# Kernel optimization log

Hardware: AMD Instinct MI355X
Metric: run time of the kernel (lower is better)

The kernel has to match this reference:

```python
import jax, jax.numpy as jnp
import numpy as np

N_NODES = 50000


def _degree_norms(edge_index, n_nodes):
    # PyG GCNConv: add self-loops, deg = 1 + in-degree at target (col)
    src, dst = edge_index[0], edge_index[1]
    deg = 1.0 + jax.ops.segment_sum(jnp.ones(src.shape[0], jnp.float32), dst,
                                    num_segments=n_nodes)
    d_inv_sqrt = 1.0 / jnp.sqrt(deg)  # deg >= 1 always (self-loop)
    norm_e = d_inv_sqrt[src] * d_inv_sqrt[dst]   # per-edge sym norm
    norm_self = d_inv_sqrt * d_inv_sqrt          # self-loop weight
    return norm_e, norm_self


def _gcn_conv(x, W, b, src, dst, norm_e, norm_self, n_nodes):
    h = x @ W                                    # [N, F_out]
    msg = h[src] * norm_e[:, None]               # gather + scale, [E, F_out]
    agg = jax.ops.segment_sum(msg, dst, num_segments=n_nodes)
    return agg + norm_self[:, None] * h + b


def setup_inputs() -> dict:
    key = jax.random.key(0)
    ks = jax.random.split(key, 10)
    F_in, H = 128, 128
    E = 1_600_000
    x = jax.random.normal(ks[0], (N_NODES, F_in), jnp.float32)
    edge_index = jax.random.randint(ks[1], (2, E), 0, N_NODES, dtype=jnp.int64)

    def glorot(k, fi, fo):
        s = jnp.sqrt(6.0 / (fi + fo)).astype(jnp.float32)
        return jax.random.uniform(k, (fi, fo), jnp.float32, -s, s)

    return {
        "x": x,
        "edge_index": edge_index,
        "W1": glorot(ks[2], F_in, H), "b1": jnp.zeros((H,), jnp.float32),
        "W2": glorot(ks[3], H, H),    "b2": jnp.zeros((H,), jnp.float32),
        "W3": glorot(ks[4], H, H),    "b3": jnp.zeros((H,), jnp.float32),
        "W4": glorot(ks[5], H, 1),    "b4": jnp.zeros((1,), jnp.float32),
    }


def reference(x, edge_index, W1, b1, W2, b2, W3, b3, W4, b4):
    src, dst = edge_index[0], edge_index[1]
    norm_e, norm_self = _degree_norms(edge_index, N_NODES)
    h = jax.nn.relu(_gcn_conv(x, W1, b1, src, dst, norm_e, norm_self, N_NODES))
    h = jax.nn.relu(_gcn_conv(h, W2, b2, src, dst, norm_e, norm_self, N_NODES))
    h = jax.nn.relu(_gcn_conv(h, W3, b3, src, dst, norm_e, norm_self, N_NODES))
    return _gcn_conv(h, W4, b4, src, dst, norm_e, norm_self, N_NODES)
```

## Files before the change

### kernel.cpp

```cpp
#include <hip/hip_runtime.h>
#include <hip/hip_bf16.h>
#include <stdint.h>

typedef unsigned int u32;
typedef unsigned short u16;

#define F 128

typedef __attribute__((ext_vector_type(8))) short bf16x8;
typedef __attribute__((ext_vector_type(8))) u16 u16x8;
typedef __attribute__((ext_vector_type(4))) float f32x4;

__device__ __forceinline__ float bf2f(u16 v){
  union { u32 u; float f; } x; x.u = ((u32)v) << 16; return x.f;
}
__device__ __forceinline__ float bflo(u32 w){
  union { u32 u; float f; } x; x.u = w << 16; return x.f;
}
__device__ __forceinline__ float bfhi(u32 w){
  union { u32 u; float f; } x; x.u = w & 0xFFFF0000u; return x.f;
}
__device__ __forceinline__ u16 f2bf(float f){
  union { float f; u32 u; } x; x.f = f;
  u32 u = x.u;
  return (u16)((u + 0x7fffu + ((u >> 16) & 1u)) >> 16);
}

__global__ void k_flags(const u32* __restrict__ xw, const u32* __restrict__ ei,
                        int* __restrict__ flags){
  if (blockIdx.x == 0){
    u32 hit = 0;
    for (int i = threadIdx.x; i < 2048; i += 256){
      u32 e = (xw[i] >> 7) & 0xFFu;
      if (e > 160u) hit = 1;
    }
    if (hit) atomicOr(&flags[1], 1);
  } else {
    u32 v = 0;
    for (int i = threadIdx.x; i < 4096; i += 256) v |= ei[2*i + 1];
    if (v) atomicOr(&flags[0], 1);
  }
}

__launch_bounds__(256)
__global__ void k_bhist(const u32* __restrict__ w, int E, const int* __restrict__ flagp,
                        int NB, int* __restrict__ bcnt){
  __shared__ int h[256];
  int st = (*flagp) ? 1 : 2;
  int t = threadIdx.x;
  h[t] = 0;
  __syncthreads();
  int base = blockIdx.x*4096;
  #pragma unroll 4
  for (int k = 0; k < 16; k++){
    int i = base + k*256 + t;
    if (i < E){
      int d = (int)w[(size_t)(E + i)*st];
      atomicAdd(&h[d >> 8], 1);
    }
  }
  __syncthreads();
  if (t < NB && h[t]) atomicAdd(&bcnt[t], h[t]);
}

__global__ void k_bscan(const int* __restrict__ bcnt, int NB, int E,
                        int* __restrict__ bbase, int* __restrict__ bump){
  __shared__ int s[256];
  int t = threadIdx.x;
  int v = (t < NB) ? bcnt[t] : 0;
  s[t] = v;
  __syncthreads();
  for (int off = 1; off < 256; off <<= 1){
    int x = (t >= off) ? s[t - off] : 0;
    __syncthreads();
    s[t] += x;
    __syncthreads();
  }
  bbase[t] = s[t] - v;
  if (t == 255) bbase[256] = E;
  bump[t] = 0;
}

__launch_bounds__(256)
__global__ void k_msplit(const u32* __restrict__ w, int E, const int* __restrict__ flagp,
                         const int* __restrict__ bbase, int* __restrict__ bump,
                         u32* __restrict__ ebuf){
  __shared__ int h[256];
  __shared__ int cb[256];
  int st = (*flagp) ? 1 : 2;
  int t = threadIdx.x;
  h[t] = 0;
  __syncthreads();
  int base = blockIdx.x*4096;
  u32 ps[16]; int bk[16]; int rk[16];
  #pragma unroll 4
  for (int k = 0; k < 16; k++){
    int i = base + k*256 + t;
    if (i < E){
      u32 s = w[(size_t)i*st];
      u32 d = w[(size_t)(E + i)*st];
      bk[k] = (int)(d >> 8);
      ps[k] = (s & 0xFFFFu) | ((d & 0xFFu) << 16);
      rk[k] = atomicAdd(&h[bk[k]], 1);
    } else bk[k] = -1;
  }
  __syncthreads();
  cb[t] = h[t] ? (bbase[t] + atomicAdd(&bump[t], h[t])) : 0;
  __syncthreads();
  #pragma unroll 4
  for (int k = 0; k < 16; k++){
    if (bk[k] >= 0) ebuf[cb[bk[k]] + rk[k]] = ps[k];
  }
}

__launch_bounds__(256)
__global__ void k_bemit(const u32* __restrict__ ebuf, const int* __restrict__ bbase,
                        int N, int* __restrict__ deg, int* __restrict__ rs,
                        u16* __restrict__ csr, float* __restrict__ dis){
  __shared__ int nd[256];
  __shared__ int nofs[256];
  __shared__ int s[256];
  int b = blockIdx.x;
  int t = threadIdx.x;
  int e0 = bbase[b], e1 = bbase[b + 1];
  nd[t] = 0;
  __syncthreads();
  for (int i = e0 + t; i < e1; i += 256) atomicAdd(&nd[ebuf[i] >> 16], 1);
  __syncthreads();
  int v = nd[t];
  s[t] = v;
  __syncthreads();
  for (int off = 1; off < 256; off <<= 1){
    int x = (t >= off) ? s[t - off] : 0;
    __syncthreads();
    s[t] += x;
    __syncthreads();
  }
  nofs[t] = s[t] - v;
  int node = b*256 + t;
  if (node < N){
    deg[node] = v;
    rs[node]  = e0 + nofs[t];
    dis[node] = rsqrtf(1.0f + (float)v);
  }
  nd[t] = 0;
  __syncthreads();
  for (int i = e0 + t; i < e1; i += 256){
    u32 p = ebuf[i];
    int d = (int)(p >> 16);
    int pos = e0 + nofs[d] + atomicAdd(&nd[d], 1);
    csr[pos] = (u16)(p & 0xFFFFu);
  }
}

__global__ void k_prep(const void* b1, const void* b2, const void* b3,
                       const void* W4, const void* b4, const int* __restrict__ isf32,
                       float* __restrict__ bb, float* __restrict__ wf4,
                       float* __restrict__ bb4){
  int t = threadIdx.x;
  int f32 = *isf32;
  if (t < 384){
    const void* s = (t < 128) ? b1 : ((t < 256) ? b2 : b3);
    int i = t & 127;
    bb[t] = f32 ? ((const float*)s)[i] : bf2f(((const u16*)s)[i]);
  } else if (t < 512){
    int i = t - 384;
    wf4[i] = f32 ? ((const float*)W4)[i] : bf2f(((const u16*)W4)[i]);
  } else if (t == 512){
    bb4[0] = f32 ? ((const float*)b4)[0] : bf2f(((const u16*)b4)[0]);
  }
}

__global__ void k_cvt_b(const void* __restrict__ in, const int* __restrict__ isf32,
                        u16* __restrict__ out, int NF8){
  int i = blockIdx.x*256 + threadIdx.x;
  if (i >= NF8) return;
  u16x8 o;
  if (*isf32){
    const f32x4* p = (const f32x4*)in + i*2;
    f32x4 v0 = p[0], v1 = p[1];
    #pragma unroll
    for (int k = 0; k < 4; k++){ o[k] = f2bf(v0[k]); o[k+4] = f2bf(v1[k]); }
  } else {
    o = *((const u16x8*)in + i);
  }
  __builtin_nontemporal_store(o, (u16x8*)out + i);
}

__global__ void k_swz3(const void* W1, const void* W2, const void* W3,
                       const int* __restrict__ isf32, u16* __restrict__ WL){
  int l = blockIdx.x >> 6;
  const void* W = (l == 0) ? W1 : ((l == 1) ? W2 : W3);
  int idx = (blockIdx.x & 63)*256 + threadIdx.x;
  int j    = idx & 7;
  int lane = (idx >> 3) & 63;
  int kb   = (idx >> 9) & 3;
  int ct   = idx >> 11;
  int m = lane & 15, q = lane >> 4;
  int k = kb*32 + q*8 + j;
  int c = ct*16 + m;
  float v = (*isf32) ? ((const float*)W)[k*F + c] : bf2f(((const u16*)W)[k*F + c]);
  WL[l*16384 + idx] = f2bf(v);
}

__launch_bounds__(256)
__global__ void k_mm(const u16* __restrict__ X, const u16* __restrict__ WL,
                     const float* __restrict__ dis, u16* __restrict__ G, int N){
  int w = threadIdx.x >> 6, lane = threadIdx.x & 63;
  int m = lane & 15, q = lane >> 4;
  int row0 = blockIdx.x*64 + w*16;
  int arow = row0 + m;
  bf16x8 a[4];
  if (arow < N){
    const u16* xp = X + (size_t)arow*F;
    #pragma unroll
    for (int kb = 0; kb < 4; kb++) a[kb] = *(const bf16x8*)(xp + kb*32 + q*8);
  } else {
    #pragma unroll
    for (int kb = 0; kb < 4; kb++) a[kb] = (bf16x8){0,0,0,0,0,0,0,0};
  }
  f32x4 acc[8];
  #pragma unroll
  for (int ct = 0; ct < 8; ct++) acc[ct] = (f32x4){0.f,0.f,0.f,0.f};
  #pragma unroll
  for (int ct = 0; ct < 8; ct++){
    #pragma unroll
    for (int kb = 0; kb < 4; kb++){
      bf16x8 b = *(const bf16x8*)(WL + ((size_t)((ct*4 + kb)*64 + lane))*8);
      acc[ct] = __builtin_amdgcn_mfma_f32_16x16x32_bf16(a[kb], b, acc[ct], 0, 0, 0);
    }
  }
  int rbase = row0 + q*4;
  #pragma unroll
  for (int r = 0; r < 4; r++){
    int row = rbase + r;
    if (row < N){
      float dv = dis[row];
      #pragma unroll
      for (int ct = 0; ct < 8; ct++)
        __builtin_nontemporal_store(f2bf(dv*acc[ct][r]),
                                    &G[(size_t)row*F + ct*16 + m]);
    }
  }
}

__launch_bounds__(256)
__global__ void k_agg(const u16* __restrict__ G, const float* __restrict__ dis,
                      const int* __restrict__ rs, const int* __restrict__ deg,
                      const u16* __restrict__ csr, const float* __restrict__ bias,
                      u16* __restrict__ Xout, int N, int relu){
  int wid  = blockIdx.x*4 + (threadIdx.x >> 6);
  int lane = threadIdx.x & 63;
  if (wid >= N) return;
  int base = rs[wid], len = deg[wid];
  const char* Gb = (const char*)G;
  u32 fo = 4u*(u32)lane;
  u32 sw = *(const u32*)(Gb + ((size_t)(u32)wid << 8) + fo);
  float a0 = bflo(sw), a1 = bfhi(sw);
  float pa[8], qa[8];
  #pragma unroll
  for (int k = 0; k < 8; k++){ pa[k] = 0.f; qa[k] = 0.f; }

  int mm = (len < 64) ? len : 64;
  u32 soff = 0;
  if (lane < mm) soff = ((u32)csr[base + lane]) << 8;
  int c0 = 0;
  while (c0 < len){
    int nxt = c0 + 64;
    u32 soff_n = 0;
    int nmm = len - nxt;
    if (nmm > 64) nmm = 64;
    if (nmm > 0 && lane < nmm) soff_n = ((u32)csr[base + nxt + lane]) << 8;
    int j = 0;
    for (; j + 8 <= mm; j += 8){
      u32 w[8];
      #pragma unroll
      for (int k = 0; k < 8; k++){
        u32 o = (u32)__builtin_amdgcn_readlane((int)soff, j + k);
        w[k] = *(const u32*)(Gb + o + fo);
      }
      #pragma unroll
      for (int k = 0; k < 8; k++){
        pa[k] += bflo(w[k]); qa[k] += bfhi(w[k]);
      }
    }
    for (; j < mm; j++){
      u32 o = (u32)__builtin_amdgcn_readlane((int)soff, j);
      u32 wv = *(const u32*)(Gb + o + fo);
      pa[0] += bflo(wv); qa[0] += bfhi(wv);
    }
    soff = soff_n; mm = nmm; c0 = nxt;
  }
  a0 += ((pa[0] + pa[1]) + (pa[2] + pa[3])) + ((pa[4] + pa[5]) + (pa[6] + pa[7]));
  a1 += ((qa[0] + qa[1]) + (qa[2] + qa[3])) + ((qa[4] + qa[5]) + (qa[6] + qa[7]));
  float dv = dis[wid];
  float o0 = fmaf(dv, a0, bias[2*lane]);
  float o1 = fmaf(dv, a1, bias[2*lane + 1]);
  if (relu){ o0 = fmaxf(o0, 0.f); o1 = fmaxf(o1, 0.f); }
  u32 pk = (u32)f2bf(o0) | ((u32)f2bf(o1) << 16);
  __builtin_nontemporal_store(pk, (u32*)(Xout + (size_t)wid*F + 2*lane));
}

__global__ void k_mm4(const u16* __restrict__ X, const float* __restrict__ W4f,
                      const float* __restrict__ dis, float* __restrict__ G4, int N){
  int gt   = blockIdx.x*blockDim.x + threadIdx.x;
  int wid  = gt >> 6;
  int lane = threadIdx.x & 63;
  if (wid >= N) return;
  u32 xw = *(const u32*)(X + (size_t)wid*F + 2*lane);
  float acc = bflo(xw)*W4f[2*lane] + bfhi(xw)*W4f[2*lane + 1];
  #pragma unroll
  for (int off = 32; off > 0; off >>= 1) acc += __shfl_down(acc, off, 64);
  if (lane == 0) G4[wid] = dis[wid]*acc;
}

__global__ void k_agg4(const float* __restrict__ G4, const float* __restrict__ dis,
                       const int* __restrict__ rs, const int* __restrict__ deg,
                       const u16* __restrict__ csr, const float* __restrict__ b4f,
                       const int* __restrict__ isf32, void* __restrict__ out, int N){
  int i = blockIdx.x*blockDim.x + threadIdx.x;
  if (i >= N) return;
  int base = rs[i], len = deg[i];
  float a0 = 0.f, a1 = 0.f, a2 = 0.f, a3 = 0.f;
  int j = 0;
  for (; j + 4 <= len; j += 4){
    int s0 = csr[base + j],     s1 = csr[base + j + 1];
    int s2 = csr[base + j + 2], s3 = csr[base + j + 3];
    a0 += G4[s0]; a1 += G4[s1]; a2 += G4[s2]; a3 += G4[s3];
  }
  for (; j < len; j++) a0 += G4[csr[base + j]];
  float r = dis[i]*(G4[i] + ((a0 + a1) + (a2 + a3))) + b4f[0];
  if (*isf32) ((float*)out)[i] = r;
  else        ((u16*)out)[i]   = f2bf(r);
}

extern "C" void kernel_launch(void* const* d_in, const int* in_sizes, int n_in,
                              void* d_out, int out_size, void* d_ws, size_t ws_size,
                              hipStream_t stream){
  const void* x0 = d_in[0];
  const u32*  ei = (const u32*)d_in[1];
  const void* Wp[4] = {d_in[2], d_in[4], d_in[6], d_in[8]};
  const void* bp[4] = {d_in[3], d_in[5], d_in[7], d_in[9]};
  int N = in_sizes[0] / F;
  int E = in_sizes[1] / 2;
  int NB = (N + 255) >> 8;

  char* base = (char*)d_ws;
  size_t off = 0;
  auto alloc = [&](size_t bytes)->char*{
    char* p = base + off;
    off = (off + bytes + 255) & ~(size_t)255;
    return p;
  };
  int*   deg  = (int*)  alloc((size_t)N*4);
  float* dis  = (float*)alloc((size_t)N*4);
  int*   rs   = (int*)  alloc((size_t)N*4);
  float* g4   = (float*)alloc((size_t)N*4);
  int*   bcnt = (int*)  alloc(1024);
  int*   bbase= (int*)  alloc(1056);
  int*   bump = (int*)  alloc(1024);
  int*   flags= (int*)  alloc(256);
  u32*   ebuf = (u32*)  alloc((size_t)E*4);
  u16*   csr  = (u16*)  alloc((size_t)E*2);
  u16*   WL   = (u16*)  alloc(3*16384*2);
  float* wf4  = (float*)alloc(F*4);
  float* bb   = (float*)alloc(3*F*4);
  float* bb4  = (float*)alloc(256);
  u16*   gbuf = (u16*)  alloc((size_t)N*F*2);
  u16*   xbuf = (u16*)  alloc((size_t)N*F*2);

  hipMemsetAsync(bcnt, 0, 1024, stream);
  hipMemsetAsync(flags, 0, 256, stream);

  int* eflag = flags + 0;
  int* isf32 = flags + 1;

  int nbt = (N + 255)/256;
  int etb = (E + 4095)/4096;

  k_flags <<<2, 256, 0, stream>>>((const u32*)x0, ei, flags);
  k_bhist <<<etb, 256, 0, stream>>>(ei, E, eflag, NB, bcnt);
  k_bscan <<<1, 256, 0, stream>>>(bcnt, NB, E, bbase, bump);
  k_msplit<<<etb, 256, 0, stream>>>(ei, E, eflag, bbase, bump, ebuf);
  k_bemit <<<NB, 256, 0, stream>>>(ebuf, bbase, N, deg, rs, csr, dis);
  k_prep  <<<1, 640, 0, stream>>>(bp[0], bp[1], bp[2], Wp[3], bp[3], isf32, bb, wf4, bb4);
  k_swz3  <<<192, 256, 0, stream>>>(Wp[0], Wp[1], Wp[2], isf32, WL);
  int NF8 = N*F/8;
  k_cvt_b <<<(NF8 + 255)/256, 256, 0, stream>>>(x0, isf32, xbuf, NF8);

  int mmb = (N + 63)/64;
  int agb = (N + 3)/4;

  for (int l = 0; l < 3; l++){
    k_mm <<<mmb, 256, 0, stream>>>(xbuf, WL + l*16384, dis, gbuf, N);
    k_agg<<<agb, 256, 0, stream>>>(gbuf, dis, rs, deg, csr, bb + l*F, xbuf, N, 1);
  }
  k_mm4 <<<((size_t)N*64 + 255)/256, 256, 0, stream>>>(xbuf, wf4, dis, g4, N);
  k_agg4<<<nbt, 256, 0, stream>>>(g4, dis, rs, deg, csr, bb4, isf32, (void*)d_out, N);
}
```

Before: 369.7 us.

## Fuse setup kernels, pad CSR rows to 16, and fold input conversion into first matmul

```diff
diff --git a/kernel.cpp b/kernel.cpp
--- a/kernel.cpp
+++ b/kernel.cpp
@@ -13,40 +13,77 @@
 
 __device__ __forceinline__ float bf2f(u16 v){
   union { u32 u; float f; } x; x.u = ((u32)v) << 16; return x.f;
-}
-__device__ __forceinline__ float bflo(u32 w){
-  union { u32 u; float f; } x; x.u = w << 16; return x.f;
-}
-__device__ __forceinline__ float bfhi(u32 w){
-  union { u32 u; float f; } x; x.u = w & 0xFFFF0000u; return x.f;
 }
 __device__ __forceinline__ u16 f2bf(float f){
   union { float f; u32 u; } x; x.f = f;
   u32 u = x.u;
   return (u16)((u + 0x7fffu + ((u >> 16) & 1u)) >> 16);
 }
-
-__global__ void k_flags(const u32* __restrict__ xw, const u32* __restrict__ ei,
-                        int* __restrict__ flags){
-  if (blockIdx.x == 0){
-    u32 hit = 0;
-    for (int i = threadIdx.x; i < 2048; i += 256){
-      u32 e = (xw[i] >> 7) & 0xFFu;
-      if (e > 160u) hit = 1;
-    }
-    if (hit) atomicOr(&flags[1], 1);
+__device__ __forceinline__ bf16x8 as_bf(u16x8 v){
+  union { u16x8 a; bf16x8 b; } u; u.a = v; return u.b;
+}
+__device__ __forceinline__ void d2(float& a, u32 w, u32 sel){
+  asm("v_dot2_f32_bf16 %0, %1, %2, %0" : "+v"(a) : "v"(w), "v"(sel));
+}
+__device__ __forceinline__ int detect_f32(const u32* xw){
+  u32 hit = 0;
+  for (int i = threadIdx.x; i < 2048; i += 256){
+    u32 e = (xw[i] >> 7) & 0xFFu;
+    if (e > 160u) hit = 1;
+  }
+  return __syncthreads_or((int)hit);
+}
+__device__ __forceinline__ int detect_stride(const u32* ei){
+  u32 v = 0;
+  for (int i = threadIdx.x; i < 4096; i += 256) v |= ei[2*i + 1];
+  return __syncthreads_or((int)v) ? 1 : 2;
+}
+
+__global__ void k_setup(const void* x0,
+                        const void* b1, const void* b2, const void* b3,
+                        const void* W1, const void* W2, const void* W3,
+                        const void* W4, const void* b4,
+                        float* __restrict__ bb, float* __restrict__ wf4,
+                        float* __restrict__ bb4, u16* __restrict__ WL,
+                        int* __restrict__ bcnt, int* __restrict__ bump,
+                        float* __restrict__ g4, u16* __restrict__ gz, int N){
+  int t = threadIdx.x, b = blockIdx.x;
+  int f32 = detect_f32((const u32*)x0);
+  if (b == 0){
+    bcnt[t] = 0; bump[t] = 0;
+    for (int i = t; i < 384; i += 256){
+      const void* s = (i < 128) ? b1 : ((i < 256) ? b2 : b3);
+      int ii = i & 127;
+      bb[i] = f32 ? ((const float*)s)[ii] : bf2f(((const u16*)s)[ii]);
+    }
+    if (t < 128) wf4[t] = f32 ? ((const float*)W4)[t] : bf2f(((const u16*)W4)[t]);
+    if (t == 0){
+      bb4[0] = f32 ? ((const float*)b4)[0] : bf2f(((const u16*)b4)[0]);
+      g4[N] = 0.f;
+    }
+    if (t < 64) ((u32*)gz)[t] = 0;
   } else {
-    u32 v = 0;
-    for (int i = threadIdx.x; i < 4096; i += 256) v |= ei[2*i + 1];
-    if (v) atomicOr(&flags[0], 1);
+    int bb_ = b - 1;
+    int l = bb_ >> 6;
+    const void* W = (l == 0) ? W1 : ((l == 1) ? W2 : W3);
+    int idx = (bb_ & 63)*256 + t;
+    int j    = idx & 7;
+    int lane = (idx >> 3) & 63;
+    int kb   = (idx >> 9) & 3;
+    int ct   = idx >> 11;
+    int m = lane & 15, q = lane >> 4;
+    int k = kb*32 + q*8 + j;
+    int c = ct*16 + m;
+    float v = f32 ? ((const float*)W)[k*F + c] : bf2f(((const u16*)W)[k*F + c]);
+    WL[l*16384 + idx] = f2bf(v);
   }
 }
 
 __launch_bounds__(256)
-__global__ void k_bhist(const u32* __restrict__ w, int E, const int* __restrict__ flagp,
-                        int NB, int* __restrict__ bcnt){
+__global__ void k_bhist(const u32* __restrict__ w, int E, int NB,
+                        int* __restrict__ bcnt){
   __shared__ int h[256];
-  int st = (*flagp) ? 1 : 2;
+  int st = detect_stride(w);
   int t = threadIdx.x;
   h[t] = 0;
   __syncthreads();
@@ -63,34 +100,26 @@
   if (t < NB && h[t]) atomicAdd(&bcnt[t], h[t]);
 }
 
-__global__ void k_bscan(const int* __restrict__ bcnt, int NB, int E,
-                        int* __restrict__ bbase, int* __restrict__ bump){
-  __shared__ int s[256];
-  int t = threadIdx.x;
-  int v = (t < NB) ? bcnt[t] : 0;
-  s[t] = v;
-  __syncthreads();
-  for (int off = 1; off < 256; off <<= 1){
-    int x = (t >= off) ? s[t - off] : 0;
-    __syncthreads();
-    s[t] += x;
-    __syncthreads();
-  }
-  bbase[t] = s[t] - v;
-  if (t == 255) bbase[256] = E;
-  bump[t] = 0;
-}
-
 __launch_bounds__(256)
-__global__ void k_msplit(const u32* __restrict__ w, int E, const int* __restrict__ flagp,
-                         const int* __restrict__ bbase, int* __restrict__ bump,
+__global__ void k_msplit(const u32* __restrict__ w, int E, int NB,
+                         const int* __restrict__ bcnt, int* __restrict__ bump,
                          u32* __restrict__ ebuf){
   __shared__ int h[256];
   __shared__ int cb[256];
-  int st = (*flagp) ? 1 : 2;
+  __shared__ int sc[256];
+  int st = detect_stride(w);
   int t = threadIdx.x;
+  int vv = (t < NB) ? bcnt[t] : 0;
+  sc[t] = vv;
   h[t] = 0;
   __syncthreads();
+  for (int off = 1; off < 256; off <<= 1){
+    int x = (t >= off) ? sc[t - off] : 0;
+    __syncthreads();
+    sc[t] += x;
+    __syncthreads();
+  }
+  int bbase = sc[t] - vv;
   int base = blockIdx.x*4096;
   u32 ps[16]; int bk[16]; int rk[16];
   #pragma unroll 4
@@ -105,7 +134,7 @@
     } else bk[k] = -1;
   }
   __syncthreads();
-  cb[t] = h[t] ? (bbase[t] + atomicAdd(&bump[t], h[t])) : 0;
+  cb[t] = h[t] ? (bbase + atomicAdd(&bump[t], h[t])) : 0;
   __syncthreads();
   #pragma unroll 4
   for (int k = 0; k < 16; k++){
@@ -114,21 +143,17 @@
 }
 
 __launch_bounds__(256)
-__global__ void k_bemit(const u32* __restrict__ ebuf, const int* __restrict__ bbase,
-                        int N, int* __restrict__ deg, int* __restrict__ rs,
-                        u16* __restrict__ csr, float* __restrict__ dis){
+__global__ void k_bemit(const u32* __restrict__ ebuf, const int* __restrict__ bcnt,
+                        int NB, int N, int* __restrict__ deg, int* __restrict__ rs,
+                        u32* __restrict__ csr32, float* __restrict__ dis){
   __shared__ int nd[256];
   __shared__ int nofs[256];
   __shared__ int s[256];
+  __shared__ int e01[2];
   int b = blockIdx.x;
   int t = threadIdx.x;
-  int e0 = bbase[b], e1 = bbase[b + 1];
-  nd[t] = 0;
-  __syncthreads();
-  for (int i = e0 + t; i < e1; i += 256) atomicAdd(&nd[ebuf[i] >> 16], 1);
-  __syncthreads();
-  int v = nd[t];
-  s[t] = v;
+  int vv = (t < NB) ? bcnt[t] : 0;
+  s[t] = vv;
   __syncthreads();
   for (int off = 1; off < 256; off <<= 1){
     int x = (t >= off) ? s[t - off] : 0;
@@ -136,11 +161,28 @@
     s[t] += x;
     __syncthreads();
   }
-  nofs[t] = s[t] - v;
+  if (t == 0){ e01[0] = (b == 0) ? 0 : s[b - 1]; e01[1] = s[b]; }
+  nd[t] = 0;
+  __syncthreads();
+  int e0 = e01[0], e1 = e01[1];
+  int pb = ((e0 + 15) & ~15) + b*4096;
+  for (int i = e0 + t; i < e1; i += 256) atomicAdd(&nd[ebuf[i] >> 16], 1);
+  __syncthreads();
+  int v = nd[t];
+  int pv = (v + 15) & ~15;
+  s[t] = pv;
+  __syncthreads();
+  for (int off = 1; off < 256; off <<= 1){
+    int x = (t >= off) ? s[t - off] : 0;
+    __syncthreads();
+    s[t] += x;
+    __syncthreads();
+  }
+  nofs[t] = s[t] - pv;
   int node = b*256 + t;
   if (node < N){
     deg[node] = v;
-    rs[node]  = e0 + nofs[t];
+    rs[node]  = pb + nofs[t];
     dis[node] = rsqrtf(1.0f + (float)v);
   }
   nd[t] = 0;
@@ -148,76 +190,49 @@
   for (int i = e0 + t; i < e1; i += 256){
     u32 p = ebuf[i];
     int d = (int)(p >> 16);
-    int pos = e0 + nofs[d] + atomicAdd(&nd[d], 1);
-    csr[pos] = (u16)(p & 0xFFFFu);
-  }
-}
-
-__global__ void k_prep(const void* b1, const void* b2, const void* b3,
-                       const void* W4, const void* b4, const int* __restrict__ isf32,
-                       float* __restrict__ bb, float* __restrict__ wf4,
-                       float* __restrict__ bb4){
-  int t = threadIdx.x;
-  int f32 = *isf32;
-  if (t < 384){
-    const void* s = (t < 128) ? b1 : ((t < 256) ? b2 : b3);
-    int i = t & 127;
-    bb[t] = f32 ? ((const float*)s)[i] : bf2f(((const u16*)s)[i]);
-  } else if (t < 512){
-    int i = t - 384;
-    wf4[i] = f32 ? ((const float*)W4)[i] : bf2f(((const u16*)W4)[i]);
-  } else if (t == 512){
-    bb4[0] = f32 ? ((const float*)b4)[0] : bf2f(((const u16*)b4)[0]);
-  }
-}
-
-__global__ void k_cvt_b(const void* __restrict__ in, const int* __restrict__ isf32,
-                        u16* __restrict__ out, int NF8){
-  int i = blockIdx.x*256 + threadIdx.x;
-  if (i >= NF8) return;
-  u16x8 o;
-  if (*isf32){
-    const f32x4* p = (const f32x4*)in + i*2;
-    f32x4 v0 = p[0], v1 = p[1];
-    #pragma unroll
-    for (int k = 0; k < 4; k++){ o[k] = f2bf(v0[k]); o[k+4] = f2bf(v1[k]); }
-  } else {
-    o = *((const u16x8*)in + i);
-  }
-  __builtin_nontemporal_store(o, (u16x8*)out + i);
-}
-
-__global__ void k_swz3(const void* W1, const void* W2, const void* W3,
-                       const int* __restrict__ isf32, u16* __restrict__ WL){
-  int l = blockIdx.x >> 6;
-  const void* W = (l == 0) ? W1 : ((l == 1) ? W2 : W3);
-  int idx = (blockIdx.x & 63)*256 + threadIdx.x;
-  int j    = idx & 7;
-  int lane = (idx >> 3) & 63;
-  int kb   = (idx >> 9) & 3;
-  int ct   = idx >> 11;
-  int m = lane & 15, q = lane >> 4;
-  int k = kb*32 + q*8 + j;
-  int c = ct*16 + m;
-  float v = (*isf32) ? ((const float*)W)[k*F + c] : bf2f(((const u16*)W)[k*F + c]);
-  WL[l*16384 + idx] = f2bf(v);
+    int pos = pb + nofs[d] + atomicAdd(&nd[d], 1);
+    csr32[pos] = (p & 0xFFFFu) << 8;
+  }
+  u32 zv = ((u32)N) << 8;
+  int bme = pb + nofs[t];
+  for (int rr = v; rr < pv; rr++) csr32[bme + rr] = zv;
 }
 
 __launch_bounds__(256)
-__global__ void k_mm(const u16* __restrict__ X, const u16* __restrict__ WL,
-                     const float* __restrict__ dis, u16* __restrict__ G, int N){
+__global__ void k_mm(const u16* __restrict__ X, const void* __restrict__ Xraw,
+                     const u16* __restrict__ WL, const float* __restrict__ dis,
+                     u16* __restrict__ G, int N, int mode){
+  int f32 = 0;
+  if (mode) f32 = detect_f32((const u32*)Xraw);
   int w = threadIdx.x >> 6, lane = threadIdx.x & 63;
   int m = lane & 15, q = lane >> 4;
   int row0 = blockIdx.x*64 + w*16;
   int arow = row0 + m;
-  bf16x8 a[4];
+  u16x8 a[4];
   if (arow < N){
-    const u16* xp = X + (size_t)arow*F;
-    #pragma unroll
-    for (int kb = 0; kb < 4; kb++) a[kb] = *(const bf16x8*)(xp + kb*32 + q*8);
+    if (mode == 0){
+      const u16* xp = X + (size_t)arow*F;
+      #pragma unroll
+      for (int kb = 0; kb < 4; kb++) a[kb] = *(const u16x8*)(xp + kb*32 + q*8);
+    } else if (f32){
+      const float* xp = (const float*)Xraw + (size_t)arow*F;
+      #pragma unroll
+      for (int kb = 0; kb < 4; kb++){
+        f32x4 v0 = *(const f32x4*)(xp + kb*32 + q*8);
+        f32x4 v1 = *(const f32x4*)(xp + kb*32 + q*8 + 4);
+        u16x8 o;
+        #pragma unroll
+        for (int k = 0; k < 4; k++){ o[k] = f2bf(v0[k]); o[k+4] = f2bf(v1[k]); }
+        a[kb] = o;
+      }
+    } else {
+      const u16* xp = (const u16*)Xraw + (size_t)arow*F;
+      #pragma unroll
+      for (int kb = 0; kb < 4; kb++) a[kb] = *(const u16x8*)(xp + kb*32 + q*8);
+    }
   } else {
     #pragma unroll
-    for (int kb = 0; kb < 4; kb++) a[kb] = (bf16x8){0,0,0,0,0,0,0,0};
+    for (int kb = 0; kb < 4; kb++) a[kb] = (u16x8){0,0,0,0,0,0,0,0};
   }
   f32x4 acc[8];
   #pragma unroll
@@ -226,8 +241,8 @@
   for (int ct = 0; ct < 8; ct++){
     #pragma unroll
     for (int kb = 0; kb < 4; kb++){
-      bf16x8 b = *(const bf16x8*)(WL + ((size_t)((ct*4 + kb)*64 + lane))*8);
-      acc[ct] = __builtin_amdgcn_mfma_f32_16x16x32_bf16(a[kb], b, acc[ct], 0, 0, 0);
+      bf16x8 bfr = *(const bf16x8*)(WL + ((size_t)((ct*4 + kb)*64 + lane))*8);
+      acc[ct] = __builtin_amdgcn_mfma_f32_16x16x32_bf16(as_bf(a[kb]), bfr, acc[ct], 0, 0, 0);
     }
   }
   int rbase = row0 + q*4;
@@ -247,32 +262,32 @@
 __launch_bounds__(256)
 __global__ void k_agg(const u16* __restrict__ G, const float* __restrict__ dis,
                       const int* __restrict__ rs, const int* __restrict__ deg,
-                      const u16* __restrict__ csr, const float* __restrict__ bias,
+                      const u32* __restrict__ csr32, const float* __restrict__ bias,
                       u16* __restrict__ Xout, int N, int relu){
   int wid  = blockIdx.x*4 + (threadIdx.x >> 6);
   int lane = threadIdx.x & 63;
   if (wid >= N) return;
-  int base = rs[wid], len = deg[wid];
+  int base = rs[wid];
+  int plen = (deg[wid] + 15) & ~15;
   const char* Gb = (const char*)G;
   u32 fo = 4u*(u32)lane;
-  u32 sw = *(const u32*)(Gb + ((size_t)(u32)wid << 8) + fo);
-  float a0 = bflo(sw), a1 = bfhi(sw);
+  u32 sel_lo = 0x00003F80u, sel_hi = 0x3F800000u;
+  u32 sw = *(const u32*)(Gb + (((size_t)(u32)wid) << 8) + fo);
   float pa[8], qa[8];
   #pragma unroll
   for (int k = 0; k < 8; k++){ pa[k] = 0.f; qa[k] = 0.f; }
-
-  int mm = (len < 64) ? len : 64;
-  u32 soff = 0;
-  if (lane < mm) soff = ((u32)csr[base + lane]) << 8;
+  d2(pa[0], sw, sel_lo); d2(qa[0], sw, sel_hi);
+
+  int mm = (plen < 64) ? plen : 64;
+  u32 soff = csr32[base + lane];
   int c0 = 0;
-  while (c0 < len){
+  while (c0 < plen){
     int nxt = c0 + 64;
+    int nmm = plen - nxt;
+    if (nmm > 64) nmm = 64;
     u32 soff_n = 0;
-    int nmm = len - nxt;
-    if (nmm > 64) nmm = 64;
-    if (nmm > 0 && lane < nmm) soff_n = ((u32)csr[base + nxt + lane]) << 8;
-    int j = 0;
-    for (; j + 8 <= mm; j += 8){
+    if (nmm > 0) soff_n = csr32[base + nxt + lane];
+    for (int j = 0; j + 8 <= mm; j += 8){
       u32 w[8];
       #pragma unroll
       for (int k = 0; k < 8; k++){
@@ -281,18 +296,13 @@
       }
       #pragma unroll
       for (int k = 0; k < 8; k++){
-        pa[k] += bflo(w[k]); qa[k] += bfhi(w[k]);
+        d2(pa[k], w[k], sel_lo); d2(qa[k], w[k], sel_hi);
       }
     }
-    for (; j < mm; j++){
-      u32 o = (u32)__builtin_amdgcn_readlane((int)soff, j);
-      u32 wv = *(const u32*)(Gb + o + fo);
-      pa[0] += bflo(wv); qa[0] += bfhi(wv);
-    }
     soff = soff_n; mm = nmm; c0 = nxt;
   }
-  a0 += ((pa[0] + pa[1]) + (pa[2] + pa[3])) + ((pa[4] + pa[5]) + (pa[6] + pa[7]));
-  a1 += ((qa[0] + qa[1]) + (qa[2] + qa[3])) + ((qa[4] + qa[5]) + (qa[6] + qa[7]));
+  float a0 = ((pa[0] + pa[1]) + (pa[2] + pa[3])) + ((pa[4] + pa[5]) + (pa[6] + pa[7]));
+  float a1 = ((qa[0] + qa[1]) + (qa[2] + qa[3])) + ((qa[4] + qa[5]) + (qa[6] + qa[7]));
   float dv = dis[wid];
   float o0 = fmaf(dv, a0, bias[2*lane]);
   float o1 = fmaf(dv, a1, bias[2*lane + 1]);
@@ -308,30 +318,34 @@
   int lane = threadIdx.x & 63;
   if (wid >= N) return;
   u32 xw = *(const u32*)(X + (size_t)wid*F + 2*lane);
-  float acc = bflo(xw)*W4f[2*lane] + bfhi(xw)*W4f[2*lane + 1];
+  float acc = bf2f((u16)xw)*W4f[2*lane] + bf2f((u16)(xw >> 16))*W4f[2*lane + 1];
   #pragma unroll
   for (int off = 32; off > 0; off >>= 1) acc += __shfl_down(acc, off, 64);
   if (lane == 0) G4[wid] = dis[wid]*acc;
 }
 
-__global__ void k_agg4(const float* __restrict__ G4, const float* __restrict__ dis,
-                       const int* __restrict__ rs, const int* __restrict__ deg,
-                       const u16* __restrict__ csr, const float* __restrict__ b4f,
-                       const int* __restrict__ isf32, void* __restrict__ out, int N){
+__global__ void k_agg4(const void* __restrict__ x0, const float* __restrict__ G4,
+                       const float* __restrict__ dis, const int* __restrict__ rs,
+                       const int* __restrict__ deg, const u32* __restrict__ csr32,
+                       const float* __restrict__ b4f, void* __restrict__ out, int N){
+  int f32 = detect_f32((const u32*)x0);
   int i = blockIdx.x*blockDim.x + threadIdx.x;
   if (i >= N) return;
-  int base = rs[i], len = deg[i];
+  int base = rs[i];
+  int plen = (deg[i] + 15) & ~15;
+  const char* Gb = (const char*)G4;
   float a0 = 0.f, a1 = 0.f, a2 = 0.f, a3 = 0.f;
-  int j = 0;
-  for (; j + 4 <= len; j += 4){
-    int s0 = csr[base + j],     s1 = csr[base + j + 1];
-    int s2 = csr[base + j + 2], s3 = csr[base + j + 3];
-    a0 += G4[s0]; a1 += G4[s1]; a2 += G4[s2]; a3 += G4[s3];
-  }
-  for (; j < len; j++) a0 += G4[csr[base + j]];
+  for (int j = 0; j < plen; j += 4){
+    u32 e0 = csr32[base + j],     e1 = csr32[base + j + 1];
+    u32 e2 = csr32[base + j + 2], e3 = csr32[base + j + 3];
+    a0 += *(const float*)(Gb + (e0 >> 6));
+    a1 += *(const float*)(Gb + (e1 >> 6));
+    a2 += *(const float*)(Gb + (e2 >> 6));
+    a3 += *(const float*)(Gb + (e3 >> 6));
+  }
   float r = dis[i]*(G4[i] + ((a0 + a1) + (a2 + a3))) + b4f[0];
-  if (*isf32) ((float*)out)[i] = r;
-  else        ((u16*)out)[i]   = f2bf(r);
+  if (f32) ((float*)out)[i] = r;
+  else     ((u16*)out)[i]   = f2bf(r);
 }
 
 extern "C" void kernel_launch(void* const* d_in, const int* in_sizes, int n_in,
@@ -355,46 +369,37 @@
   int*   deg  = (int*)  alloc((size_t)N*4);
   float* dis  = (float*)alloc((size_t)N*4);
   int*   rs   = (int*)  alloc((size_t)N*4);
-  float* g4   = (float*)alloc((size_t)N*4);
+  float* g4   = (float*)alloc((size_t)(N+1)*4);
   int*   bcnt = (int*)  alloc(1024);
-  int*   bbase= (int*)  alloc(1056);
   int*   bump = (int*)  alloc(1024);
-  int*   flags= (int*)  alloc(256);
   u32*   ebuf = (u32*)  alloc((size_t)E*4);
-  u16*   csr  = (u16*)  alloc((size_t)E*2);
+  u32*   csr32= (u32*)  alloc(((size_t)E + (size_t)(NB+1)*4096 + 128)*4);
   u16*   WL   = (u16*)  alloc(3*16384*2);
   float* wf4  = (float*)alloc(F*4);
   float* bb   = (float*)alloc(3*F*4);
   float* bb4  = (float*)alloc(256);
-  u16*   gbuf = (u16*)  alloc((size_t)N*F*2);
+  u16*   gbuf = (u16*)  alloc((size_t)(N+1)*F*2);
   u16*   xbuf = (u16*)  alloc((size_t)N*F*2);
-
-  hipMemsetAsync(bcnt, 0, 1024, stream);
-  hipMemsetAsync(flags, 0, 256, stream);
-
-  int* eflag = flags + 0;
-  int* isf32 = flags + 1;
 
   int nbt = (N + 255)/256;
   int etb = (E + 4095)/4096;
 
-  k_flags <<<2, 256, 0, stream>>>((const u32*)x0, ei, flags);
-  k_bhist <<<etb, 256, 0, stream>>>(ei, E, eflag, NB, bcnt);
-  k_bscan <<<1, 256, 0, stream>>>(bcnt, NB, E, bbase, bump);
-  k_msplit<<<etb, 256, 0, stream>>>(ei, E, eflag, bbase, bump, ebuf);
-  k_bemit <<<NB, 256, 0, stream>>>(ebuf, bbase, N, deg, rs, csr, dis);
-  k_prep  <<<1, 640, 0, stream>>>(bp[0], bp[1], bp[2], Wp[3], bp[3], isf32, bb, wf4, bb4);
-  k_swz3  <<<192, 256, 0, stream>>>(Wp[0], Wp[1], Wp[2], isf32, WL);
-  int NF8 = N*F/8;
-  k_cvt_b <<<(NF8 + 255)/256, 256, 0, stream>>>(x0, isf32, xbuf, NF8);
+  k_setup<<<193, 256, 0, stream>>>(x0, bp[0], bp[1], bp[2],
+                                   Wp[0], Wp[1], Wp[2], Wp[3], bp[3],
+                                   bb, wf4, bb4, WL, bcnt, bump, g4,
+                                   gbuf + (size_t)N*F, N);
+  k_bhist <<<etb, 256, 0, stream>>>(ei, E, NB, bcnt);
+  k_msplit<<<etb, 256, 0, stream>>>(ei, E, NB, bcnt, bump, ebuf);
+  k_bemit <<<NB, 256, 0, stream>>>(ebuf, bcnt, NB, N, deg, rs, csr32, dis);
 
   int mmb = (N + 63)/64;
   int agb = (N + 3)/4;
 
   for (int l = 0; l < 3; l++){
-    k_mm <<<mmb, 256, 0, stream>>>(xbuf, WL + l*16384, dis, gbuf, N);
-    k_agg<<<agb, 256, 0, stream>>>(gbuf, dis, rs, deg, csr, bb + l*F, xbuf, N, 1);
+    k_mm <<<mmb, 256, 0, stream>>>(xbuf, (l == 0) ? x0 : (const void*)xbuf,
+                                   WL + l*16384, dis, gbuf, N, (l == 0) ? 1 : 0);
+    k_agg<<<agb, 256, 0, stream>>>(gbuf, dis, rs, deg, csr32, bb + l*F, xbuf, N, 1);
   }
   k_mm4 <<<((size_t)N*64 + 255)/256, 256, 0, stream>>>(xbuf, wf4, dis, g4, N);
-  k_agg4<<<nbt, 256, 0, stream>>>(g4, dis, rs, deg, csr, bb4, isf32, (void*)d_out, N);
-}
+  k_agg4<<<nbt, 256, 0, stream>>>(x0, g4, dis, rs, deg, csr32, bb4, (void*)d_out, N);
+}
```

Result: slower. 383.7 us (+3.8%).
